# Optimization experiments

Hardware: AMD Instinct MI355X
Metric: run time of the kernel (lower is better)

Reference implementation:

```python
import jax, jax.numpy as jnp
import numpy as np

B, S, ENC = 16, 1500, 1280      # batch, audio frames, encoder dim
K = 2                            # pool stride -> in_dim = ENC*K
IN_DIM = ENC * K                 # 2560
LLM = 2048                       # output dim
HID = 512                        # expert hidden dim
E, TOPK = 8, 2                   # num experts, top-k
EPS = 1e-6


def _ln(x, g, b):
    m = jnp.mean(x, -1, keepdims=True)
    v = jnp.mean((x - m) ** 2, -1, keepdims=True)
    return (x - m) * jax.lax.rsqrt(v + EPS) * g + b


def _swiglu(x, w12, w3):
    # w12: [2H, D], w3: [O, H]; dropout is identity at inference
    h = x @ w12.T
    gate, val = jnp.split(h, 2, axis=-1)
    return (jax.nn.silu(gate) * val) @ w3.T


def setup_inputs() -> dict:
    key = jax.random.key(0)
    ks = jax.random.split(key, 12)
    sc = 0.02
    return {
        "x": jax.random.normal(ks[0], (B, S, ENC), jnp.float32),
        "ln_pre_g": 1.0 + sc * jax.random.normal(ks[1], (IN_DIM,), jnp.float32),
        "ln_pre_b": sc * jax.random.normal(ks[2], (IN_DIM,), jnp.float32),
        "router_w": sc * jax.random.normal(ks[3], (E, IN_DIM), jnp.float32),
        "router_b": sc * jax.random.normal(ks[4], (E,), jnp.float32),
        "shared_w12": sc * jax.random.normal(ks[5], (2 * HID, IN_DIM), jnp.float32),
        "shared_w3": sc * jax.random.normal(ks[6], (LLM, HID), jnp.float32),
        "experts_w12": sc * jax.random.normal(ks[7], (E, 2 * HID, IN_DIM), jnp.float32),
        "experts_w3": sc * jax.random.normal(ks[8], (E, LLM, HID), jnp.float32),
        "ln_post_g": 1.0 + sc * jax.random.normal(ks[9], (LLM,), jnp.float32),
        "ln_post_b": sc * jax.random.normal(ks[10], (LLM,), jnp.float32),
    }


def reference(x, ln_pre_g, ln_pre_b, router_w, router_b,
              shared_w12, shared_w3, experts_w12, experts_w3,
              ln_post_g, ln_post_b):
    b, s, d = x.shape
    pad = (-s) % K
    if pad:
        x = jnp.pad(x, ((0, 0), (0, pad), (0, 0)))
    xk = x.reshape(b, -1, d * K)          # [B, S/K, IN_DIM]
    new_s = xk.shape[1]
    nx = _ln(xk.reshape(-1, d * K), ln_pre_g, ln_pre_b)   # [T, IN_DIM]

    shared = _swiglu(nx, shared_w12, shared_w3)            # [T, LLM]

    logits = nx @ router_w.T + router_b                    # [T, E]
    probs = jax.nn.softmax(logits, -1)
    w, idx = jax.lax.top_k(probs, TOPK)                    # [T, K]
    w = w / (jnp.sum(w, -1, keepdims=True) + 1e-20)
    # combine[t, e] = sum_k w[t,k] * (idx[t,k]==e)  (equiv to masked loop + scatter-add)
    combine = jnp.sum(jax.nn.one_hot(idx, E, dtype=nx.dtype) * w[..., None], axis=1)  # [T, E]

    hid = jnp.einsum('td,efd->tef', nx, experts_w12)       # [T, E, 2H]
    gate, val = jnp.split(hid, 2, axis=-1)
    act = jax.nn.silu(gate) * val                          # [T, E, H]
    eo = jnp.einsum('teh,eoh->teo', act, experts_w3)       # [T, E, LLM]
    routed = jnp.einsum('teo,te->to', eo, combine)         # [T, LLM]

    out = _ln(shared + routed, ln_post_g, ln_post_b)
    return out.reshape(b, new_s, LLM)
```

## Files before the change

kernel.cpp:

```cpp
#include <hip/hip_runtime.h>

#define T_TOK 12000
#define NSLOT 24000
#define DIN 2560
#define DH 512
#define DOUT 2048
#define NEXP 8
#define MSH 12000
#define SHBASE 24000

typedef unsigned short u16;
typedef unsigned int u32;
typedef __attribute__((ext_vector_type(4))) float f32x4;
typedef __attribute__((ext_vector_type(8))) short short8;
typedef __attribute__((ext_vector_type(4))) u16 u16x4;
typedef __attribute__((ext_vector_type(8))) u16 u16x8;

__device__ __forceinline__ u16 f2bf(float f) {
  u32 u = __builtin_bit_cast(u32, f);
  return (u16)((u + 0x7fffu + ((u >> 16) & 1u)) >> 16);
}
__device__ __forceinline__ float bf2f(u16 h) {
  return __builtin_bit_cast(float, (u32)h << 16);
}

__device__ __forceinline__ void gload_lds16(const void* g, void* l) {
  __builtin_amdgcn_global_load_lds((const __attribute__((address_space(1))) u32*)g,
                                   (__attribute__((address_space(3))) u32*)l, 16, 0, 0);
}

#define CN0 655360
#define CN1 262144
#define CN2 5242880
#define CN3 2097152
__global__ __launch_bounds__(256) void cvt4_kernel(
    const float* __restrict__ s0, u16* __restrict__ d0,
    const float* __restrict__ s1, u16* __restrict__ d1,
    const float* __restrict__ s2, u16* __restrict__ d2,
    const float* __restrict__ s3, u16* __restrict__ d3) {
  int i = blockIdx.x * 256 + threadIdx.x;
  const float* s; u16* d;
  if (i < CN0) { s = s0; d = d0; }
  else if (i < CN0 + CN1) { i -= CN0; s = s1; d = d1; }
  else if (i < CN0 + CN1 + CN2) { i -= CN0 + CN1; s = s2; d = d2; }
  else { i -= CN0 + CN1 + CN2; if (i >= CN3) return; s = s3; d = d3; }
  f32x4 v = ((const f32x4*)s)[i];
  u16x4 o = { f2bf(v.x), f2bf(v.y), f2bf(v.z), f2bf(v.w) };
  ((u16x4*)d)[i] = o;
}

__global__ __launch_bounds__(256) void ln_router_kernel(
    const float* __restrict__ x, const float* __restrict__ gamma, const float* __restrict__ beta,
    const float* __restrict__ rw, const float* __restrict__ rb,
    u16* __restrict__ nx, int* __restrict__ tok_e, float* __restrict__ tok_w,
    int* __restrict__ count) {
  const int tid = threadIdx.x;
  const int t = blockIdx.x * 4 + (tid >> 6);
  const int lane = tid & 63;
  const f32x4* xrow = (const f32x4*)(x + (size_t)t * DIN);

  __shared__ float rwl[NEXP][256];

  f32x4 xv[10];
  float s = 0.f, s2 = 0.f;
#pragma unroll
  for (int c = 0; c < 10; ++c) {
    xv[c] = xrow[c * 64 + lane];
#pragma unroll
    for (int i = 0; i < 4; ++i) { s += xv[c][i]; s2 += xv[c][i] * xv[c][i]; }
  }
#pragma unroll
  for (int off = 32; off > 0; off >>= 1) {
    s += __shfl_xor(s, off);
    s2 += __shfl_xor(s2, off);
  }
  const float mean = s * (1.0f / DIN);
  const float var = s2 * (1.0f / DIN) - mean * mean;
  const float rstd = rsqrtf(var + 1e-6f);

  u16* nxrow = nx + (size_t)t * DIN;
#pragma unroll
  for (int c = 0; c < 10; ++c) {
    f32x4 g = ((const f32x4*)gamma)[c * 64 + lane];
    f32x4 b = ((const f32x4*)beta)[c * 64 + lane];
    xv[c] = (xv[c] - mean) * rstd * g + b;
    u16x4 p = { f2bf(xv[c].x), f2bf(xv[c].y), f2bf(xv[c].z), f2bf(xv[c].w) };
    ((u16x4*)nxrow)[c * 64 + lane] = p;
  }

  float lp[NEXP];
#pragma unroll
  for (int e = 0; e < NEXP; ++e) lp[e] = 0.f;
#pragma unroll
  for (int c = 0; c < 10; ++c) {
    __syncthreads();
#pragma unroll
    for (int e = 0; e < NEXP; ++e) rwl[e][tid] = rw[(size_t)e * DIN + c * 256 + tid];
    __syncthreads();
#pragma unroll
    for (int e = 0; e < NEXP; ++e) {
      f32x4 r = *(const f32x4*)&rwl[e][lane * 4];
      lp[e] += xv[c].x * r.x + xv[c].y * r.y + xv[c].z * r.z + xv[c].w * r.w;
    }
  }
#pragma unroll
  for (int e = 0; e < NEXP; ++e)
#pragma unroll
    for (int off = 32; off > 0; off >>= 1) lp[e] += __shfl_xor(lp[e], off);

  if (lane == 0) {
    float lg[NEXP];
#pragma unroll
    for (int e = 0; e < NEXP; ++e) lg[e] = lp[e] + rb[e];
    float mx = lg[0];
#pragma unroll
    for (int e = 1; e < NEXP; ++e) mx = fmaxf(mx, lg[e]);
    float p[NEXP], ps = 0.f;
#pragma unroll
    for (int e = 0; e < NEXP; ++e) { p[e] = expf(lg[e] - mx); ps += p[e]; }
    int i0 = 0;
#pragma unroll
    for (int e = 1; e < NEXP; ++e) if (p[e] > p[i0]) i0 = e;
    int i1 = (i0 == 0) ? 1 : 0;
#pragma unroll
    for (int e = 0; e < NEXP; ++e) if (e != i0 && p[e] > p[i1]) i1 = e;
    float w0 = p[i0] / ps, w1 = p[i1] / ps;
    const float inv = 1.0f / (w0 + w1 + 1e-20f);
    w0 *= inv; w1 *= inv;
    tok_e[2 * t] = i0; tok_e[2 * t + 1] = i1;
    tok_w[2 * t] = w0; tok_w[2 * t + 1] = w1;
    atomicAdd(&count[i0 * 32], 1);
    atomicAdd(&count[i1 * 32], 1);
  }
}

__global__ void prefix_kernel(const int* __restrict__ count, int* __restrict__ prefix) {
  if (threadIdx.x == 0) {
    int acc = 0;
    for (int e = 0; e < NEXP; ++e) { prefix[e] = acc; acc += count[e * 32]; }
  }
}

__global__ __launch_bounds__(256) void assign_kernel(
    const int* __restrict__ tok_e, const float* __restrict__ tok_w, const int* __restrict__ prefix,
    int* __restrict__ cursor, int* __restrict__ slot_token, float* __restrict__ slot_w,
    int* __restrict__ token_slot) {
  const int t = blockIdx.x * 256 + threadIdx.x;
  if (t >= T_TOK) return;
#pragma unroll
  for (int k = 0; k < 2; ++k) {
    const int e = tok_e[2 * t + k];
    const int pos = atomicAdd(&cursor[e * 32], 1);
    const int sl = prefix[e] + pos;
    slot_token[sl] = t;
    slot_w[sl] = tok_w[2 * t + k];
    token_slot[2 * t + k] = sl;
  }
}

__global__ __launch_bounds__(256, 2) void gemm_ffn1(
    const u16* __restrict__ A0, const u16* __restrict__ Bsh, const u16* __restrict__ Bex,
    u16* __restrict__ ACT,
    const int* __restrict__ cnt32, const int* __restrict__ prefix,
    const int* __restrict__ slot_token) {
  constexpr int K = 2560;
  constexpr int NX = 8;
  __shared__ u16 ldsA[128 * 64];
  __shared__ u16 ldsG[64 * 64];
  __shared__ u16 ldsV[64 * 64];

  int A_act = 0;
#pragma unroll
  for (int ee = 0; ee < 9; ++ee) {
    const int c = (ee == 8) ? MSH : cnt32[ee * 32];
    A_act += ((c + 127) >> 7) * NX;
  }
  const int bid = blockIdx.x;
  if (bid >= A_act) return;

  const int xcd = bid & 7, rank = bid >> 3;
  const int q = A_act >> 3, r = A_act & 7;
  const int tile = (xcd < r ? xcd * (q + 1) : r * (q + 1) + (xcd - r) * q) + rank;

  int e = 8, local = 0, m_valid = MSH, row_off = 0;
  {
    int bacc = 0, found = 0;
#pragma unroll
    for (int ee = 0; ee < 9; ++ee) {
      const int c = (ee == 8) ? MSH : cnt32[ee * 32];
      const int w = ((c + 127) >> 7) * NX;
      if (!found && tile < bacc + w) {
        found = 1; e = ee; local = tile - bacc; m_valid = c;
        row_off = (ee == 8) ? 0 : prefix[ee];
      }
      bacc += w;
    }
  }
  const int ty = local / NX;
  const int tx = local % NX;
  const int crow_base = (e == 8) ? SHBASE : row_off;
  const u16* Bb = (e == 8) ? Bsh : Bex + (size_t)e * 1024 * K;

  const int tid = threadIdx.x;
  const int lane = tid & 63;
  const int wid = tid >> 6;
  const int sk8 = ((lane & 7) ^ (lane >> 3)) * 8;

  const u16* aptr[4];
#pragma unroll
  for (int i = 0; i < 4; ++i) {
    const int rr = wid * 32 + i * 8 + (lane >> 3);
    int gr = ty * 128 + rr;
    gr = gr < m_valid ? gr : (m_valid - 1);
    const int ar = (e == 8) ? gr : slot_token[row_off + gr];
    aptr[i] = A0 + (size_t)ar * K;
  }
  const u16* gptr[2];
  const u16* vptr[2];
#pragma unroll
  for (int j = 0; j < 2; ++j) {
    const int rr = wid * 16 + j * 8 + (lane >> 3);
    gptr[j] = Bb + (size_t)(tx * 64 + rr) * K;
    vptr[j] = Bb + (size_t)(512 + tx * 64 + rr) * K;
  }

  const f32x4 zero = {0.f, 0.f, 0.f, 0.f};
  f32x4 accg[4][2], accv[4][2];
#pragma unroll
  for (int m = 0; m < 4; ++m)
#pragma unroll
    for (int n = 0; n < 2; ++n) { accg[m][n] = zero; accv[m][n] = zero; }

  const int wr = (wid >> 1) * 64;
  const int wc = (wid & 1) * 32;
  const int fr = lane & 15;
  const int fk = (lane >> 4) * 8;

  for (int k0 = 0; k0 < K; k0 += 64) {
#pragma unroll
    for (int i = 0; i < 4; ++i)
      gload_lds16(aptr[i] + k0 + sk8, &ldsA[(wid * 4 + i) * 512]);
#pragma unroll
    for (int j = 0; j < 2; ++j) {
      gload_lds16(gptr[j] + k0 + sk8, &ldsG[(wid * 2 + j) * 512]);
      gload_lds16(vptr[j] + k0 + sk8, &ldsV[(wid * 2 + j) * 512]);
    }
    __syncthreads();
#pragma unroll
    for (int kk = 0; kk < 2; ++kk) {
      short8 af[4], bg[2], bv[2];
      const int kbs = (kk * 32 + fk) ^ ((lane & 7) << 3);
#pragma unroll
      for (int m = 0; m < 4; ++m)
        af[m] = *(const short8*)&ldsA[(wr + m * 16 + fr) * 64 + kbs];
#pragma unroll
      for (int n = 0; n < 2; ++n) {
        bg[n] = *(const short8*)&ldsG[(wc + n * 16 + fr) * 64 + kbs];
        bv[n] = *(const short8*)&ldsV[(wc + n * 16 + fr) * 64 + kbs];
      }
#pragma unroll
      for (int m = 0; m < 4; ++m)
#pragma unroll
        for (int n = 0; n < 2; ++n) {
          accg[m][n] = __builtin_amdgcn_mfma_f32_16x16x32_bf16(af[m], bg[n], accg[m][n], 0, 0, 0);
          accv[m][n] = __builtin_amdgcn_mfma_f32_16x16x32_bf16(af[m], bv[n], accv[m][n], 0, 0, 0);
        }
    }
    __syncthreads();
  }

  const int ccol = tx * 64 + wc + (lane & 15);
#pragma unroll
  for (int m = 0; m < 4; ++m) {
#pragma unroll
    for (int i = 0; i < 4; ++i) {
      const int row = wr + m * 16 + (lane >> 4) * 4 + i;
      const int gr = ty * 128 + row;
      if (gr < m_valid) {
        u16* crow = ACT + (size_t)(crow_base + gr) * DH;
#pragma unroll
        for (int n = 0; n < 2; ++n) {
          const float g = accg[m][n][i];
          const float v = accv[m][n][i];
          const float sig = 1.0f / (1.0f + __expf(-g));
          crow[ccol + n * 16] = f2bf(g * sig * v);
        }
      }
    }
  }
}

__global__ __launch_bounds__(256, 2) void gemm_ffn2(
    const u16* __restrict__ A0, const u16* __restrict__ Bsh, const u16* __restrict__ Bex,
    u16* __restrict__ C,
    const int* __restrict__ cnt32, const int* __restrict__ prefix,
    const float* __restrict__ slot_w) {
  constexpr int N = 2048;
  constexpr int K = 512;
  constexpr int NX = 16;
  __shared__ u16 ldsA[128 * 64];
  __shared__ u16 ldsB[128 * 64];

  int A_act = 0;
#pragma unroll
  for (int ee = 0; ee < 9; ++ee) {
    const int c = (ee == 8) ? MSH : cnt32[ee * 32];
    A_act += ((c + 127) >> 7) * NX;
  }
  const int bid = blockIdx.x;
  if (bid >= A_act) return;

  const int xcd = bid & 7, rank = bid >> 3;
  const int q = A_act >> 3, r = A_act & 7;
  const int tile = (xcd < r ? xcd * (q + 1) : r * (q + 1) + (xcd - r) * q) + rank;

  int e = 8, local = 0, m_valid = MSH, row_off = 0;
  {
    int bacc = 0, found = 0;
#pragma unroll
    for (int ee = 0; ee < 9; ++ee) {
      const int c = (ee == 8) ? MSH : cnt32[ee * 32];
      const int w = ((c + 127) >> 7) * NX;
      if (!found && tile < bacc + w) {
        found = 1; e = ee; local = tile - bacc; m_valid = c;
        row_off = (ee == 8) ? 0 : prefix[ee];
      }
      bacc += w;
    }
  }
  const int ty = local / NX;
  const int tx = local % NX;
  const int crow_base = (e == 8) ? SHBASE : row_off;
  const u16* Bb = (e == 8) ? Bsh : Bex + (size_t)e * N * K;

  const int tid = threadIdx.x;
  const int lane = tid & 63;
  const int wid = tid >> 6;
  const int sk8 = ((lane & 7) ^ (lane >> 3)) * 8;

  const u16* aptr[4];
  const u16* bptr[4];
#pragma unroll
  for (int i = 0; i < 4; ++i) {
    const int rr = wid * 32 + i * 8 + (lane >> 3);
    int gr = ty * 128 + rr;
    gr = gr < m_valid ? gr : (m_valid - 1);
    aptr[i] = A0 + (size_t)(crow_base + gr) * K;
    bptr[i] = Bb + (size_t)(tx * 128 + rr) * K;
  }

  const f32x4 zero = {0.f, 0.f, 0.f, 0.f};
  f32x4 acc[4][4];
#pragma unroll
  for (int m = 0; m < 4; ++m)
#pragma unroll
    for (int n = 0; n < 4; ++n) acc[m][n] = zero;

  const int wr = (wid >> 1) * 64;
  const int wc = (wid & 1) * 64;
  const int fr = lane & 15;
  const int fk = (lane >> 4) * 8;

  for (int k0 = 0; k0 < K; k0 += 64) {
#pragma unroll
    for (int i = 0; i < 4; ++i) {
      gload_lds16(aptr[i] + k0 + sk8, &ldsA[(wid * 4 + i) * 512]);
      gload_lds16(bptr[i] + k0 + sk8, &ldsB[(wid * 4 + i) * 512]);
    }
    __syncthreads();
#pragma unroll
    for (int kk = 0; kk < 2; ++kk) {
      short8 af[4], bfm[4];
      const int kbs = (kk * 32 + fk) ^ ((lane & 7) << 3);
#pragma unroll
      for (int m = 0; m < 4; ++m)
        af[m] = *(const short8*)&ldsA[(wr + m * 16 + fr) * 64 + kbs];
#pragma unroll
      for (int n = 0; n < 4; ++n)
        bfm[n] = *(const short8*)&ldsB[(wc + n * 16 + fr) * 64 + kbs];
#pragma unroll
      for (int m = 0; m < 4; ++m)
#pragma unroll
        for (int n = 0; n < 4; ++n)
          acc[m][n] = __builtin_amdgcn_mfma_f32_16x16x32_bf16(af[m], bfm[n], acc[m][n], 0, 0, 0);
    }
    __syncthreads();
  }

  const int ccol = wc + (lane & 15);
#pragma unroll
  for (int m = 0; m < 4; ++m) {
#pragma unroll
    for (int i = 0; i < 4; ++i) {
      const int row = wr + m * 16 + (lane >> 4) * 4 + i;
      const int gr = ty * 128 + row;
      if (gr < m_valid) {
        const float wscale = (e == 8) ? 1.0f : slot_w[row_off + gr];
        u16* crow = C + (size_t)(crow_base + gr) * N + tx * 128;
#pragma unroll
        for (int n = 0; n < 4; ++n) crow[ccol + n * 16] = f2bf(acc[m][n][i] * wscale);
      }
    }
  }
}

__global__ __launch_bounds__(256) void final_ln_kernel(
    const u16* __restrict__ O16, const int* __restrict__ token_slot,
    const float* __restrict__ gamma, const float* __restrict__ beta, float* __restrict__ out) {
  const int t = blockIdx.x * 4 + (threadIdx.x >> 6);
  const int lane = threadIdx.x & 63;
  const int s0 = token_slot[2 * t], s1 = token_slot[2 * t + 1];
  const u16* rsh = O16 + (size_t)(SHBASE + t) * DOUT;
  const u16* r0 = O16 + (size_t)s0 * DOUT;
  const u16* r1 = O16 + (size_t)s1 * DOUT;

  float v[32];
  float s = 0.f, s2 = 0.f;
#pragma unroll
  for (int c = 0; c < 4; ++c) {
    const int col = c * 512 + lane * 8;
    u16x8 a8 = *(const u16x8*)&rsh[col];
    u16x8 b8 = *(const u16x8*)&r0[col];
    u16x8 c8 = *(const u16x8*)&r1[col];
#pragma unroll
    for (int i = 0; i < 8; ++i) {
      const float x = bf2f(a8[i]) + bf2f(b8[i]) + bf2f(c8[i]);
      v[c * 8 + i] = x;
      s += x;
      s2 += x * x;
    }
  }
#pragma unroll
  for (int off = 32; off > 0; off >>= 1) {
    s += __shfl_xor(s, off);
    s2 += __shfl_xor(s2, off);
  }
  const float mean = s * (1.0f / DOUT);
  const float var = s2 * (1.0f / DOUT) - mean * mean;
  const float rstd = rsqrtf(var + 1e-6f);

  float* orow = out + (size_t)t * DOUT;
#pragma unroll
  for (int c = 0; c < 4; ++c) {
    const int col = c * 512 + lane * 8;
    f32x4 g0 = ((const f32x4*)gamma)[col >> 2], g1 = ((const f32x4*)gamma)[(col >> 2) + 1];
    f32x4 b0 = ((const f32x4*)beta)[col >> 2],  b1 = ((const f32x4*)beta)[(col >> 2) + 1];
    f32x4 o0, o1;
#pragma unroll
    for (int i = 0; i < 4; ++i) {
      o0[i] = (v[c * 8 + i] - mean) * rstd * g0[i] + b0[i];
      o1[i] = (v[c * 8 + 4 + i] - mean) * rstd * g1[i] + b1[i];
    }
    *(f32x4*)&orow[col] = o0;
    *(f32x4*)&orow[col + 4] = o1;
  }
}

extern "C" void kernel_launch(void* const* d_in, const int* in_sizes, int n_in,
                              void* d_out, int out_size, void* d_ws, size_t ws_size,
                              hipStream_t stream) {
  (void)in_sizes; (void)n_in; (void)out_size; (void)ws_size;
  const float* x = (const float*)d_in[0];
  const float* ln_pre_g = (const float*)d_in[1];
  const float* ln_pre_b = (const float*)d_in[2];
  const float* router_w = (const float*)d_in[3];
  const float* router_b = (const float*)d_in[4];
  const float* shared_w12 = (const float*)d_in[5];
  const float* shared_w3 = (const float*)d_in[6];
  const float* experts_w12 = (const float*)d_in[7];
  const float* experts_w3 = (const float*)d_in[8];
  const float* ln_post_g = (const float*)d_in[9];
  const float* ln_post_b = (const float*)d_in[10];
  float* out = (float*)d_out;

  size_t off = 0;
  char* ws = (char*)d_ws;
  auto take = [&](size_t bytes) -> void* {
    void* p = ws + off;
    off += (bytes + 255) & ~(size_t)255;
    return p;
  };
  u16* w12s = (u16*)take((size_t)1024 * 2560 * 2);
  u16* w3s  = (u16*)take((size_t)2048 * 512 * 2);
  u16* ew12 = (u16*)take((size_t)NEXP * 1024 * 2560 * 2);
  u16* ew3  = (u16*)take((size_t)NEXP * 2048 * 512 * 2);
  u16* nx   = (u16*)take((size_t)T_TOK * DIN * 2);
  u16* act  = (u16*)take((size_t)36000 * DH * 2);
  u16* O16  = (u16*)take((size_t)36000 * DOUT * 2);
  int* tok_e = (int*)take(NSLOT * 4);
  float* tok_w = (float*)take(NSLOT * 4);
  int* slot_token = (int*)take(NSLOT * 4);
  float* slot_w = (float*)take(NSLOT * 4);
  int* token_slot = (int*)take(NSLOT * 4);
  int* cnt = (int*)take(3 * 8 * 32 * 4);
  int* cursor = cnt + 8 * 32;
  int* prefix = cnt + 2 * 8 * 32;

  hipMemsetAsync(cnt, 0, 3 * 8 * 32 * 4, stream);

  cvt4_kernel<<<(CN0 + CN1 + CN2 + CN3) / 256, 256, 0, stream>>>(
      shared_w12, w12s, shared_w3, w3s, experts_w12, ew12, experts_w3, ew3);

  ln_router_kernel<<<T_TOK / 4, 256, 0, stream>>>(x, ln_pre_g, ln_pre_b, router_w, router_b,
                                                  nx, tok_e, tok_w, cnt);
  prefix_kernel<<<1, 64, 0, stream>>>(cnt, prefix);
  assign_kernel<<<(T_TOK + 255) / 256, 256, 0, stream>>>(tok_e, tok_w, prefix, cursor,
                                                         slot_token, slot_w, token_slot);

  gemm_ffn1<<<289 * 8, 256, 0, stream>>>(nx, w12s, ew12, act, cnt, prefix, slot_token);
  gemm_ffn2<<<289 * 16, 256, 0, stream>>>(act, w3s, ew3, O16, cnt, prefix, slot_w);

  final_ln_kernel<<<T_TOK / 4, 256, 0, stream>>>(O16, token_slot, ln_post_g, ln_post_b, out);
}
```

Baseline: 534.2 us.

## Double K-tile depth in FFN2 GEMM and stage epilogue through LDS for vector stores

The FFN2 grouped GEMM now loads 128-wide K slices per iteration instead of 64, which halves the number of barrier pairs over K=512, and uses a 16-way XOR swizzle for the wider rows. The epilogue writes scaled bf16 results into a padded LDS tile and then issues coalesced 16-byte row stores instead of scattered 2-byte stores. LDS use per block grows to 64KB, which may limit occupancy under the two-blocks-per-CU launch bound.

```diff
diff --git a/kernel.cpp b/kernel.cpp
--- a/kernel.cpp
+++ b/kernel.cpp
@@ -298,8 +298,7 @@
   constexpr int N = 2048;
   constexpr int K = 512;
   constexpr int NX = 16;
-  __shared__ u16 ldsA[128 * 64];
-  __shared__ u16 ldsB[128 * 64];
+  __shared__ u16 ldsbuf[2 * 128 * 128];
 
   int A_act = 0;
 #pragma unroll
@@ -336,17 +335,17 @@
   const int tid = threadIdx.x;
   const int lane = tid & 63;
   const int wid = tid >> 6;
-  const int sk8 = ((lane & 7) ^ (lane >> 3)) * 8;
-
-  const u16* aptr[4];
-  const u16* bptr[4];
-#pragma unroll
-  for (int i = 0; i < 4; ++i) {
-    const int rr = wid * 32 + i * 8 + (lane >> 3);
+
+  const u16* aptr[8];
+  const u16* bptr[8];
+#pragma unroll
+  for (int i = 0; i < 8; ++i) {
+    const int rr = (wid * 8 + i) * 4 + (lane >> 4);
+    const int sg = ((lane & 15) ^ (rr & 15)) * 8;
     int gr = ty * 128 + rr;
     gr = gr < m_valid ? gr : (m_valid - 1);
-    aptr[i] = A0 + (size_t)(crow_base + gr) * K;
-    bptr[i] = Bb + (size_t)(tx * 128 + rr) * K;
+    aptr[i] = A0 + (size_t)(crow_base + gr) * K + sg;
+    bptr[i] = Bb + (size_t)(tx * 128 + rr) * K + sg;
   }
 
   const f32x4 zero = {0.f, 0.f, 0.f, 0.f};
@@ -359,25 +358,24 @@
   const int wr = (wid >> 1) * 64;
   const int wc = (wid & 1) * 64;
   const int fr = lane & 15;
-  const int fk = (lane >> 4) * 8;
-
-  for (int k0 = 0; k0 < K; k0 += 64) {
-#pragma unroll
-    for (int i = 0; i < 4; ++i) {
-      gload_lds16(aptr[i] + k0 + sk8, &ldsA[(wid * 4 + i) * 512]);
-      gload_lds16(bptr[i] + k0 + sk8, &ldsB[(wid * 4 + i) * 512]);
+
+  for (int k0 = 0; k0 < K; k0 += 128) {
+#pragma unroll
+    for (int i = 0; i < 8; ++i) {
+      gload_lds16(aptr[i] + k0, &ldsbuf[(wid * 8 + i) * 512]);
+      gload_lds16(bptr[i] + k0, &ldsbuf[16384 + (wid * 8 + i) * 512]);
     }
     __syncthreads();
 #pragma unroll
-    for (int kk = 0; kk < 2; ++kk) {
+    for (int kk = 0; kk < 4; ++kk) {
       short8 af[4], bfm[4];
-      const int kbs = (kk * 32 + fk) ^ ((lane & 7) << 3);
+      const int so = ((kk * 4 + (lane >> 4)) ^ fr) * 8;
 #pragma unroll
       for (int m = 0; m < 4; ++m)
-        af[m] = *(const short8*)&ldsA[(wr + m * 16 + fr) * 64 + kbs];
+        af[m] = *(const short8*)&ldsbuf[(wr + m * 16 + fr) * 128 + so];
 #pragma unroll
       for (int n = 0; n < 4; ++n)
-        bfm[n] = *(const short8*)&ldsB[(wc + n * 16 + fr) * 64 + kbs];
+        bfm[n] = *(const short8*)&ldsbuf[16384 + (wc + n * 16 + fr) * 128 + so];
 #pragma unroll
       for (int m = 0; m < 4; ++m)
 #pragma unroll
@@ -387,19 +385,30 @@
     __syncthreads();
   }
 
-  const int ccol = wc + (lane & 15);
+  u16* ldsT = ldsbuf;
 #pragma unroll
   for (int m = 0; m < 4; ++m) {
 #pragma unroll
     for (int i = 0; i < 4; ++i) {
       const int row = wr + m * 16 + (lane >> 4) * 4 + i;
-      const int gr = ty * 128 + row;
-      if (gr < m_valid) {
-        const float wscale = (e == 8) ? 1.0f : slot_w[row_off + gr];
-        u16* crow = C + (size_t)(crow_base + gr) * N + tx * 128;
-#pragma unroll
-        for (int n = 0; n < 4; ++n) crow[ccol + n * 16] = f2bf(acc[m][n][i] * wscale);
-      }
+      int gr = ty * 128 + row;
+      gr = gr < m_valid ? gr : (m_valid - 1);
+      const float wscale = (e == 8) ? 1.0f : slot_w[row_off + gr];
+#pragma unroll
+      for (int n = 0; n < 4; ++n)
+        ldsT[row * 144 + wc + n * 16 + (lane & 15)] = f2bf(acc[m][n][i] * wscale);
+    }
+  }
+  __syncthreads();
+  {
+    const int row = tid >> 1;
+    const int ch = (tid & 1) * 64;
+    const int gr = ty * 128 + row;
+    if (gr < m_valid) {
+      u16* crow = C + (size_t)(crow_base + gr) * N + tx * 128 + ch;
+#pragma unroll
+      for (int j = 0; j < 8; ++j)
+        *(u16x8*)&crow[j * 8] = *(const u16x8*)&ldsT[row * 144 + ch + j * 8];
     }
   }
 }
```

Result: slower. 561.5 us (+5.1%).
